# Kernel optimization log

Measured on AMD Instinct MI355X. Metric: run time of the kernel, lower is better.

The kernel has to match this reference:

```python
import jax, jax.numpy as jnp
import numpy as np

NH, DH, DM = 16, 128, 2048
ROPE_THETA = 10000.0


def setup_inputs() -> dict:
    key = jax.random.key(0)
    k1, k2, k3 = jax.random.split(key, 3)
    x = jax.random.normal(k1, (2, 2048, DM), dtype=jnp.float32)
    w_qkv = jax.random.normal(k2, (3 * DM, DM), dtype=jnp.float32) * (DM ** -0.5)
    w_op = jax.random.normal(k3, (DM, DM), dtype=jnp.float32) * (DM ** -0.5)
    return {"x": x, "w_qkv": w_qkv, "w_op": w_op}


def _rope_tables(T, dtype):
    inv_freq = 1.0 / (ROPE_THETA ** (jnp.arange(0, DH, 2, dtype=jnp.float32) / DH))
    t = jnp.arange(T, dtype=jnp.float32)
    freqs = jnp.outer(t, inv_freq)              # (T, DH/2)
    emb = jnp.concatenate([freqs, freqs], axis=-1)  # (T, DH)
    cos = jnp.cos(emb)[None, :, None, :].astype(dtype)  # (1,T,1,DH)
    sin = jnp.sin(emb)[None, :, None, :].astype(dtype)
    return cos, sin


def _rotate_half(a):
    a1, a2 = a[..., : DH // 2], a[..., DH // 2 :]
    return jnp.concatenate([-a2, a1], axis=-1)


def reference(x, w_qkv, w_op):
    B, T, D = x.shape
    qkv = jnp.einsum('btd,ed->bte', x, w_qkv).reshape(B, T, 3, NH, DH)
    q, k, v = qkv[:, :, 0], qkv[:, :, 1], qkv[:, :, 2]  # (B,T,NH,DH)

    cos, sin = _rope_tables(T, x.dtype)
    q = q * cos + _rotate_half(q) * sin
    k = k * cos + _rotate_half(k) * sin

    # causal scaled dot-product attention
    scale = 1.0 / jnp.sqrt(jnp.asarray(DH, dtype=x.dtype))
    scores = jnp.einsum('bqhd,bkhd->bhqk', q, k) * scale  # (B,NH,T,T)
    causal = jnp.tril(jnp.ones((T, T), dtype=bool))
    scores = jnp.where(causal[None, None], scores, jnp.asarray(-1e30, dtype=x.dtype))
    attn = jax.nn.softmax(scores, axis=-1)
    out = jnp.einsum('bhqk,bkhd->bqhd', attn, v).reshape(B, T, D)
    return jnp.einsum('btd,ed->bte', out, w_op)
```

## Files before the change

### kernel.cpp

```cpp
#include <hip/hip_runtime.h>
#include <hip/hip_bf16.h>
#include <cstdint>

#define NHEAD 16
#define DHEAD 128
#define DMODEL 2048
#define TSEQ 2048
#define BATCH 2

using bf16 = __hip_bfloat16;
typedef __attribute__((ext_vector_type(4))) float  f32x4;
typedef __attribute__((ext_vector_type(4))) float  float4_t;
typedef __attribute__((ext_vector_type(4))) short  s16x4;
typedef __bf16 bf16x8 __attribute__((ext_vector_type(8)));

#define GLOAD_LDS16(gptr, lptr)                                                        \
  __builtin_amdgcn_global_load_lds((const __attribute__((address_space(1))) void*)(gptr), \
                                   (__attribute__((address_space(3))) void*)(lptr), 16, 0, 0)

__device__ __forceinline__ float bf2f(bf16 v) { return __bfloat162float(v); }
__device__ __forceinline__ bf16  f2bf(float f) { return __float2bfloat16(f); }
__device__ __forceinline__ unsigned short bfbits(float f) {
  return __builtin_bit_cast(unsigned short, f2bf(f));
}
__device__ __forceinline__ unsigned int pack2(float a, float b) {
  return (unsigned int)bfbits(a) | ((unsigned int)bfbits(b) << 16);
}

__global__ void cast_f32_to_bf16(const float* __restrict__ in, unsigned short* __restrict__ out, int n4) {
  int stride = gridDim.x * blockDim.x;
  for (int i = blockIdx.x * blockDim.x + threadIdx.x; i < n4; i += stride) {
    float4_t v = reinterpret_cast<const float4_t*>(in)[i];
    s16x4 r;
    r.x = (short)bfbits(v.x);
    r.y = (short)bfbits(v.y);
    r.z = (short)bfbits(v.z);
    r.w = (short)bfbits(v.w);
    reinterpret_cast<s16x4*>(out)[i] = r;
  }
}

__global__ void rope_tables(float* __restrict__ ctab, float* __restrict__ stab) {
  int i = blockIdx.x * blockDim.x + threadIdx.x;
  if (i >= TSEQ * 64) return;
  int t = i >> 6, f = i & 63;
  float inv = __expf(-((2.0f * (float)f) / 128.0f) * logf(10000.0f));
  float ang = (float)t * inv;
  ctab[i] = cosf(ang);
  stab[i] = sinf(ang);
}

__global__ void transpose_v(const unsigned short* __restrict__ qkv, unsigned short* __restrict__ vt) {
  __shared__ short tile[64][132];
  const int bh = blockIdx.y;
  const int b = bh >> 4, h = bh & 15;
  const int t0 = blockIdx.x * 64;
  const int tid = threadIdx.x;
#pragma unroll
  for (int p = 0; p < 8; ++p) {
    int row  = p * 8 + (tid >> 5);
    int col  = (tid & 31) * 4;
    const unsigned short* src = qkv + (size_t)(b * TSEQ + t0 + row) * (3 * DMODEL) + 2 * DMODEL + h * DHEAD + col;
    s16x4 v = *reinterpret_cast<const s16x4*>(src);
    *reinterpret_cast<s16x4*>(&tile[row][col]) = v;
  }
  __syncthreads();
#pragma unroll
  for (int q = 0; q < 8; ++q) {
    int idx = q * 256 + tid;
    int d = idx >> 4, tq = idx & 15;
    s16x4 r;
    r.x = tile[tq * 4 + 0][d];
    r.y = tile[tq * 4 + 1][d];
    r.z = tile[tq * 4 + 2][d];
    r.w = tile[tq * 4 + 3][d];
    *reinterpret_cast<s16x4*>(vt + (size_t)(bh * DHEAD + d) * TSEQ + t0 + tq * 4) = r;
  }
}

__device__ __forceinline__ void store_c(float* p, float v) { *p = v; }
__device__ __forceinline__ void store_c(unsigned short* p, float v) { *p = bfbits(v); }

template <typename CT, bool ROPE>
__global__ __launch_bounds__(256, 2) void gemm_bt(const unsigned short* __restrict__ A,
                                                  const unsigned short* __restrict__ B,
                                                  CT* __restrict__ C, int M, int N, int K,
                                                  const float* __restrict__ ctab,
                                                  const float* __restrict__ stab) {
  __shared__ unsigned short As[128 * 32];
  __shared__ unsigned short Bs[128 * 32];
  const int tid  = threadIdx.x;
  const int wave = tid >> 6, lane = tid & 63;
  const int m0 = blockIdx.x * 128, n0 = blockIdx.y * 128;
  const int wm = wave * 32;
  const int lrow = lane >> 4, lcol = lane & 15;
  f32x4 acc[2][8] = {};

  for (int k0 = 0; k0 < K; k0 += 32) {
#pragma unroll
    for (int it = 0; it < 2; ++it) {
      int chunk = wave * 2 + it;
      int eoff  = chunk * 512 + lane * 8;
      int row   = eoff >> 5, col = eoff & 31;
      GLOAD_LDS16(A + (size_t)(m0 + row) * K + k0 + col, As + chunk * 512);
      GLOAD_LDS16(B + (size_t)(n0 + row) * K + k0 + col, Bs + chunk * 512);
    }
    __syncthreads();
    bf16x8 af[2], bfr[8];
#pragma unroll
    for (int mi = 0; mi < 2; ++mi)
      af[mi] = *reinterpret_cast<const bf16x8*>(&As[(wm + mi * 16 + lcol) * 32 + lrow * 8]);
#pragma unroll
    for (int ni = 0; ni < 8; ++ni)
      bfr[ni] = *reinterpret_cast<const bf16x8*>(&Bs[(ni * 16 + lcol) * 32 + lrow * 8]);
#pragma unroll
    for (int mi = 0; mi < 2; ++mi)
#pragma unroll
      for (int ni = 0; ni < 8; ++ni)
        acc[mi][ni] = __builtin_amdgcn_mfma_f32_16x16x32_bf16(af[mi], bfr[ni], acc[mi][ni], 0, 0, 0);
    __syncthreads();
  }

  if (ROPE && n0 < 2 * DMODEL) {
    const float qsc = (n0 < DMODEL) ? 0.08838834764831845f : 1.0f;
#pragma unroll
    for (int mi = 0; mi < 2; ++mi)
#pragma unroll
      for (int j = 0; j < 4; ++j) {
        const int r = m0 + wm + mi * 16 + lrow * 4 + j;
        const int t = r & (TSEQ - 1);
#pragma unroll
        for (int ni = 0; ni < 4; ++ni) {
          const int f = ni * 16 + lcol;
          const float cc = ctab[t * 64 + f];
          const float ss = stab[t * 64 + f];
          const float a1 = acc[mi][ni][j];
          const float a2 = acc[mi][ni + 4][j];
          store_c(C + (size_t)r * N + n0 + f,      (a1 * cc - a2 * ss) * qsc);
          store_c(C + (size_t)r * N + n0 + f + 64, (a2 * cc + a1 * ss) * qsc);
        }
      }
  } else {
#pragma unroll
    for (int mi = 0; mi < 2; ++mi)
#pragma unroll
      for (int ni = 0; ni < 8; ++ni)
#pragma unroll
        for (int j = 0; j < 4; ++j) {
          int r = m0 + wm + mi * 16 + lrow * 4 + j;
          int c = n0 + ni * 16 + lcol;
          store_c(C + (size_t)r * N + c, acc[mi][ni][j]);
        }
  }
}

__global__ __launch_bounds__(512, 4) void flash_attn(const unsigned short* __restrict__ qkv,
                                                     const unsigned short* __restrict__ vt,
                                                     unsigned short* __restrict__ out) {
  __shared__ unsigned short kb[2][64 * 128];
  __shared__ unsigned short vb[2][128 * 64];
  __shared__ unsigned short plds[8][16 * 64];

  const int tid  = threadIdx.x;
  const int wave = tid >> 6, lane = tid & 63;
  const int lrow = lane >> 4, lcol = lane & 15;
  const int h = blockIdx.y, b = blockIdx.z;
  const int q0b = blockIdx.x * 128;
  const int q0w = q0b + wave * 16;
  const size_t qkbase = (size_t)b * TSEQ * (3 * DMODEL);
  const unsigned short* kptr = qkv + qkbase + DMODEL + h * DHEAD;
  const unsigned short* vptr = vt + (size_t)((b * NHEAD + h) * DHEAD) * TSEQ;

  bf16x8 qf[4];
#pragma unroll
  for (int kk = 0; kk < 4; ++kk)
    qf[kk] = *reinterpret_cast<const bf16x8*>(
        qkv + qkbase + (size_t)(q0w + lcol) * (3 * DMODEL) + h * DHEAD + kk * 32 + lrow * 8);

  f32x4 o[8] = {};
  float m = -1.0e30f, l = 0.f;

  const int nsteps = 2 * blockIdx.x + 2;

#define STAGE_KV(bi, kv0s)                                                              \
  {                                                                                     \
    _Pragma("unroll")                                                                   \
    for (int c = 0; c < 2; ++c) {                                                       \
      int cc = c * 512 + tid;                                                           \
      int krow = cc >> 4, kchk = (cc & 15) ^ (krow & 7);                                \
      GLOAD_LDS16(kptr + (size_t)((kv0s) + krow) * (3 * DMODEL) + kchk * 8,             \
                  &kb[bi][cc * 8]);                                                     \
      int vrow = cc >> 3, vchk = (cc & 7) ^ (vrow & 7);                                 \
      GLOAD_LDS16(vptr + (size_t)vrow * TSEQ + (kv0s) + vchk * 8,                       \
                  &vb[bi][cc * 8]);                                                     \
    }                                                                                   \
  }

  STAGE_KV(0, 0);
  __syncthreads();

  int cur = 0;
  for (int s = 0; s < nsteps; ++s) {
    const int kv0 = s * 64;
    if (s + 1 < nsteps) STAGE_KV(cur ^ 1, kv0 + 64);

    if (kv0 <= q0w + 15) {
      const unsigned short* kbc = kb[cur];
      const unsigned short* vbc = vb[cur];

      f32x4 sc[4] = {};
      __builtin_amdgcn_s_setprio(1);
#pragma unroll
      for (int n = 0; n < 4; ++n) {
        const int r = n * 16 + lcol;
#pragma unroll
        for (int kk = 0; kk < 4; ++kk) {
          bf16x8 kf = *reinterpret_cast<const bf16x8*>(
              &kbc[r * 128 + (((kk * 4 + lrow) ^ (lcol & 7)) << 3)]);
          sc[n] = __builtin_amdgcn_mfma_f32_16x16x32_bf16(kf, qf[kk], sc[n], 0, 0, 0);
        }
      }
      __builtin_amdgcn_s_setprio(0);

      const bool diag = (kv0 + 63 > q0w);
      const int qi = q0w + lcol;
      float sv[16];
#pragma unroll
      for (int n = 0; n < 4; ++n)
#pragma unroll
        for (int j = 0; j < 4; ++j) {
          float v = sc[n][j];
          if (diag && (kv0 + n * 16 + lrow * 4 + j) > qi) v = -1.0e30f;
          sv[n * 4 + j] = v;
        }
      float t8[8];
#pragma unroll
      for (int j = 0; j < 8; ++j) t8[j] = fmaxf(sv[j], sv[j + 8]);
#pragma unroll
      for (int j = 0; j < 4; ++j) t8[j] = fmaxf(t8[j], t8[j + 4]);
      float pm = fmaxf(fmaxf(t8[0], t8[1]), fmaxf(t8[2], t8[3]));
      pm = fmaxf(pm, __shfl_xor(pm, 16));
      pm = fmaxf(pm, __shfl_xor(pm, 32));

      if (__any(pm > m + 8.f)) {
        const float mn  = fmaxf(m, pm);
        const float fsc = __expf(m - mn);
        m = mn;
        l *= fsc;
#pragma unroll
        for (int c = 0; c < 8; ++c) o[c] *= fsc;
      }

#pragma unroll
      for (int i = 0; i < 16; ++i) sv[i] = __expf(sv[i] - m);
      float a8[8];
#pragma unroll
      for (int j = 0; j < 8; ++j) a8[j] = sv[j] + sv[j + 8];
#pragma unroll
      for (int j = 0; j < 4; ++j) a8[j] += a8[j + 4];
      float rs = (a8[0] + a8[1]) + (a8[2] + a8[3]);
      rs += __shfl_xor(rs, 16);
      rs += __shfl_xor(rs, 32);
      l += rs;

      char* pw = reinterpret_cast<char*>(&plds[wave][0]);
#pragma unroll
      for (int n = 0; n < 4; ++n)
#pragma unroll
        for (int j = 0; j < 4; j += 2) {
          int boff = (lcol << 7) + ((((n << 1) + (lrow >> 1)) ^ (lcol & 7)) << 4) +
                     ((lrow & 1) << 3) + (j << 1);
          *reinterpret_cast<unsigned int*>(pw + boff) = pack2(sv[n * 4 + j], sv[n * 4 + j + 1]);
        }
      asm volatile("s_waitcnt lgkmcnt(0)" ::: "memory");

      bf16x8 pf0 = *reinterpret_cast<const bf16x8*>(
          pw + (lcol << 7) + ((lrow ^ (lcol & 7)) << 4));
      bf16x8 pf1 = *reinterpret_cast<const bf16x8*>(
          pw + (lcol << 7) + (((4 + lrow) ^ (lcol & 7)) << 4));

      __builtin_amdgcn_s_setprio(1);
#pragma unroll
      for (int c = 0; c < 8; ++c) {
        const int d = c * 16 + lcol;
        bf16x8 vf0 = *reinterpret_cast<const bf16x8*>(
            &vbc[d * 64 + ((lrow ^ (lcol & 7)) << 3)]);
        o[c] = __builtin_amdgcn_mfma_f32_16x16x32_bf16(vf0, pf0, o[c], 0, 0, 0);
        bf16x8 vf1 = *reinterpret_cast<const bf16x8*>(
            &vbc[d * 64 + (((4 + lrow) ^ (lcol & 7)) << 3)]);
        o[c] = __builtin_amdgcn_mfma_f32_16x16x32_bf16(vf1, pf1, o[c], 0, 0, 0);
      }
      __builtin_amdgcn_s_setprio(0);
    }

    __syncthreads();
    cur ^= 1;
  }

  const float rl = 1.0f / l;
  const int trow = q0w + lcol;
#pragma unroll
  for (int c = 0; c < 8; ++c) {
    s16x4 st;
#pragma unroll
    for (int j = 0; j < 4; ++j) st[j] = (short)bfbits(o[c][j] * rl);
    *reinterpret_cast<s16x4*>(
        out + (size_t)(b * TSEQ + trow) * DMODEL + h * DHEAD + c * 16 + lrow * 4) = st;
  }
#undef STAGE_KV
}

extern "C" void kernel_launch(void* const* d_in, const int* in_sizes, int n_in,
                              void* d_out, int out_size, void* d_ws, size_t ws_size,
                              hipStream_t stream) {
  const float* x     = (const float*)d_in[0];
  const float* w_qkv = (const float*)d_in[1];
  const float* w_op  = (const float*)d_in[2];
  float* out = (float*)d_out;

  const size_t SZ_XB  = (size_t)4096 * 2048 * 2;
  const size_t SZ_WQ  = (size_t)6144 * 2048 * 2;
  const size_t SZ_WO  = (size_t)2048 * 2048 * 2;
  const size_t SZ_QKV = (size_t)4096 * 6144 * 2;
  const size_t SZ_VT  = (size_t)32 * 128 * 2048 * 2;
  const size_t SZ_AO  = (size_t)4096 * 2048 * 2;
  const size_t SZ_TAB = (size_t)2048 * 64 * 4;
  const size_t NEEDED = SZ_XB + SZ_WQ + SZ_WO + SZ_QKV + SZ_VT + SZ_AO + 2 * SZ_TAB;
  if (ws_size < NEEDED) return;

  char* p = (char*)d_ws;
  unsigned short* xb   = (unsigned short*)p; p += SZ_XB;
  unsigned short* wqb  = (unsigned short*)p; p += SZ_WQ;
  unsigned short* wob  = (unsigned short*)p; p += SZ_WO;
  unsigned short* qkv  = (unsigned short*)p; p += SZ_QKV;
  unsigned short* vt   = (unsigned short*)p; p += SZ_VT;
  unsigned short* ao   = (unsigned short*)p; p += SZ_AO;
  float* ctab = (float*)p; p += SZ_TAB;
  float* stab = (float*)p; p += SZ_TAB;

  cast_f32_to_bf16<<<dim3(2048), dim3(256), 0, stream>>>(x, xb, 4096 * 2048 / 4);
  cast_f32_to_bf16<<<dim3(2048), dim3(256), 0, stream>>>(w_qkv, wqb, 6144 * 2048 / 4);
  cast_f32_to_bf16<<<dim3(2048), dim3(256), 0, stream>>>(w_op, wob, 2048 * 2048 / 4);
  rope_tables<<<dim3(512), dim3(256), 0, stream>>>(ctab, stab);

  gemm_bt<unsigned short, true><<<dim3(32, 48), dim3(256), 0, stream>>>(
      xb, wqb, qkv, 4096, 6144, 2048, ctab, stab);
  transpose_v<<<dim3(32, 32), dim3(256), 0, stream>>>(qkv, vt);
  flash_attn<<<dim3(16, 16, 2), dim3(512), 0, stream>>>(qkv, vt, ao);
  gemm_bt<float, false><<<dim3(32, 16), dim3(256), 0, stream>>>(
      ao, wob, out, 4096, 2048, 2048, nullptr, nullptr);
}
```

Measured before the change: 305.5 us.

## Replace GEMM with 4-stage pipelined, swizzled 256x128 tile kernel

```diff
diff --git a/kernel.cpp b/kernel.cpp
--- a/kernel.cpp
+++ b/kernel.cpp
@@ -82,73 +82,119 @@
 __device__ __forceinline__ void store_c(unsigned short* p, float v) { *p = bfbits(v); }
 
 template <typename CT, bool ROPE>
-__global__ __launch_bounds__(256, 2) void gemm_bt(const unsigned short* __restrict__ A,
-                                                  const unsigned short* __restrict__ B,
-                                                  CT* __restrict__ C, int M, int N, int K,
-                                                  const float* __restrict__ ctab,
-                                                  const float* __restrict__ stab) {
-  __shared__ unsigned short As[128 * 32];
-  __shared__ unsigned short Bs[128 * 32];
+__global__ __launch_bounds__(512, 2) void gemm_pipe(const unsigned short* __restrict__ A,
+                                                    const unsigned short* __restrict__ B,
+                                                    CT* __restrict__ C, int M, int N, int K,
+                                                    const float* __restrict__ ctab,
+                                                    const float* __restrict__ stab) {
+  __shared__ __align__(16) unsigned short As[4][256 * 32];
+  __shared__ __align__(16) unsigned short Bs[4][128 * 32];
+
   const int tid  = threadIdx.x;
-  const int wave = tid >> 6, lane = tid & 63;
-  const int m0 = blockIdx.x * 128, n0 = blockIdx.y * 128;
-  const int wm = wave * 32;
+  const int lane = tid & 63;
+  const int wave = tid >> 6;
   const int lrow = lane >> 4, lcol = lane & 15;
-  f32x4 acc[2][8] = {};
-
-  for (int k0 = 0; k0 < K; k0 += 32) {
-#pragma unroll
-    for (int it = 0; it < 2; ++it) {
-      int chunk = wave * 2 + it;
-      int eoff  = chunk * 512 + lane * 8;
-      int row   = eoff >> 5, col = eoff & 31;
-      GLOAD_LDS16(A + (size_t)(m0 + row) * K + k0 + col, As + chunk * 512);
-      GLOAD_LDS16(B + (size_t)(n0 + row) * K + k0 + col, Bs + chunk * 512);
+  const int wm2 = wave >> 2, wn4 = wave & 3;
+
+  const int cpx = gridDim.x >> 3;
+  const int bid = (blockIdx.x & 7) * cpx + (blockIdx.x >> 3);
+  const int nby = N >> 7;
+  const int m0 = (bid / nby) * 256;
+  const int n0 = (bid % nby) * 128;
+
+  const int NT = K >> 5;
+
+  f32x4 acc[8][2] = {};
+
+#define GSTAGE(t)                                                                       \
+  {                                                                                     \
+    const int bi_ = (t) & 3;                                                            \
+    const int k0_ = (t) << 5;                                                           \
+    _Pragma("unroll")                                                                   \
+    for (int l_ = 0; l_ < 2; ++l_) {                                                    \
+      int D_ = (l_ * 512 + tid) * 16;                                                   \
+      int R_ = D_ >> 6;                                                                 \
+      int cb_ = (D_ & 63) ^ ((R_ & 3) << 4);                                            \
+      GLOAD_LDS16(A + (size_t)(m0 + R_) * K + k0_ + (cb_ >> 1),                         \
+                  (char*)(&As[bi_][0]) + D_);                                           \
+    }                                                                                   \
+    {                                                                                   \
+      int D_ = tid * 16;                                                                \
+      int R_ = D_ >> 6;                                                                 \
+      int cb_ = (D_ & 63) ^ ((R_ & 3) << 4);                                            \
+      GLOAD_LDS16(B + (size_t)(n0 + R_) * K + k0_ + (cb_ >> 1),                         \
+                  (char*)(&Bs[bi_][0]) + D_);                                           \
+    }                                                                                   \
+  }
+
+  GSTAGE(0);
+  GSTAGE(1);
+  GSTAGE(2);
+  asm volatile("s_waitcnt vmcnt(6)" ::: "memory");
+  __builtin_amdgcn_s_barrier();
+  asm volatile("" ::: "memory");
+
+  for (int t = 0; t < NT; ++t) {
+    if (t + 3 < NT) GSTAGE(t + 3);
+
+    const char* Ab = (const char*)(&As[t & 3][0]);
+    const char* Bb = (const char*)(&Bs[t & 3][0]);
+
+    bf16x8 bfr[2];
+#pragma unroll
+    for (int ni = 0; ni < 2; ++ni) {
+      const int R = wn4 * 16 + ni * 64 + lcol;
+      bfr[ni] = *reinterpret_cast<const bf16x8*>(Bb + R * 64 + ((lrow * 16) ^ ((R & 3) << 4)));
     }
-    __syncthreads();
-    bf16x8 af[2], bfr[8];
-#pragma unroll
-    for (int mi = 0; mi < 2; ++mi)
-      af[mi] = *reinterpret_cast<const bf16x8*>(&As[(wm + mi * 16 + lcol) * 32 + lrow * 8]);
-#pragma unroll
-    for (int ni = 0; ni < 8; ++ni)
-      bfr[ni] = *reinterpret_cast<const bf16x8*>(&Bs[(ni * 16 + lcol) * 32 + lrow * 8]);
-#pragma unroll
-    for (int mi = 0; mi < 2; ++mi)
-#pragma unroll
-      for (int ni = 0; ni < 8; ++ni)
-        acc[mi][ni] = __builtin_amdgcn_mfma_f32_16x16x32_bf16(af[mi], bfr[ni], acc[mi][ni], 0, 0, 0);
-    __syncthreads();
-  }
+#pragma unroll
+    for (int mh = 0; mh < 2; ++mh) {
+      bf16x8 af[4];
+#pragma unroll
+      for (int q = 0; q < 4; ++q) {
+        const int R = wm2 * 128 + (mh * 4 + q) * 16 + lcol;
+        af[q] = *reinterpret_cast<const bf16x8*>(Ab + R * 64 + ((lrow * 16) ^ ((R & 3) << 4)));
+      }
+      __builtin_amdgcn_s_setprio(1);
+#pragma unroll
+      for (int q = 0; q < 4; ++q)
+#pragma unroll
+        for (int ni = 0; ni < 2; ++ni)
+          acc[mh * 4 + q][ni] =
+              __builtin_amdgcn_mfma_f32_16x16x32_bf16(af[q], bfr[ni], acc[mh * 4 + q][ni], 0, 0, 0);
+      __builtin_amdgcn_s_setprio(0);
+    }
+
+    asm volatile("s_waitcnt vmcnt(6)" ::: "memory");
+    __builtin_amdgcn_s_barrier();
+    asm volatile("" ::: "memory");
+  }
+#undef GSTAGE
 
   if (ROPE && n0 < 2 * DMODEL) {
     const float qsc = (n0 < DMODEL) ? 0.08838834764831845f : 1.0f;
-#pragma unroll
-    for (int mi = 0; mi < 2; ++mi)
+    const int f = wn4 * 16 + lcol;
+#pragma unroll
+    for (int mi = 0; mi < 8; ++mi)
 #pragma unroll
       for (int j = 0; j < 4; ++j) {
-        const int r = m0 + wm + mi * 16 + lrow * 4 + j;
+        const int r = m0 + wm2 * 128 + mi * 16 + lrow * 4 + j;
         const int t = r & (TSEQ - 1);
-#pragma unroll
-        for (int ni = 0; ni < 4; ++ni) {
-          const int f = ni * 16 + lcol;
-          const float cc = ctab[t * 64 + f];
-          const float ss = stab[t * 64 + f];
-          const float a1 = acc[mi][ni][j];
-          const float a2 = acc[mi][ni + 4][j];
-          store_c(C + (size_t)r * N + n0 + f,      (a1 * cc - a2 * ss) * qsc);
-          store_c(C + (size_t)r * N + n0 + f + 64, (a2 * cc + a1 * ss) * qsc);
-        }
+        const float cc = ctab[t * 64 + f];
+        const float ss = stab[t * 64 + f];
+        const float a1 = acc[mi][0][j];
+        const float a2 = acc[mi][1][j];
+        store_c(C + (size_t)r * N + n0 + f,      (a1 * cc - a2 * ss) * qsc);
+        store_c(C + (size_t)r * N + n0 + f + 64, (a2 * cc + a1 * ss) * qsc);
       }
   } else {
 #pragma unroll
-    for (int mi = 0; mi < 2; ++mi)
-#pragma unroll
-      for (int ni = 0; ni < 8; ++ni)
+    for (int mi = 0; mi < 8; ++mi)
+#pragma unroll
+      for (int ni = 0; ni < 2; ++ni)
 #pragma unroll
         for (int j = 0; j < 4; ++j) {
-          int r = m0 + wm + mi * 16 + lrow * 4 + j;
-          int c = n0 + ni * 16 + lcol;
+          const int r = m0 + wm2 * 128 + mi * 16 + lrow * 4 + j;
+          const int c = n0 + wn4 * 16 + ni * 64 + lcol;
           store_c(C + (size_t)r * N + c, acc[mi][ni][j]);
         }
   }
@@ -343,10 +389,10 @@
   cast_f32_to_bf16<<<dim3(2048), dim3(256), 0, stream>>>(w_op, wob, 2048 * 2048 / 4);
   rope_tables<<<dim3(512), dim3(256), 0, stream>>>(ctab, stab);
 
-  gemm_bt<unsigned short, true><<<dim3(32, 48), dim3(256), 0, stream>>>(
+  gemm_pipe<unsigned short, true><<<dim3(768), dim3(512), 0, stream>>>(
       xb, wqb, qkv, 4096, 6144, 2048, ctab, stab);
   transpose_v<<<dim3(32, 32), dim3(256), 0, stream>>>(qkv, vt);
   flash_attn<<<dim3(16, 16, 2), dim3(512), 0, stream>>>(qkv, vt, ao);
-  gemm_bt<float, false><<<dim3(32, 16), dim3(256), 0, stream>>>(
+  gemm_pipe<float, false><<<dim3(256), dim3(512), 0, stream>>>(
       ao, wob, out, 4096, 2048, 2048, nullptr, nullptr);
 }
```

New measurement: 370.5 us. 1.21x slower.
